# Kernel optimization log

Measured on AMD Instinct MI355X. Metric: run time of the kernel, lower is better.

## Reference

```python
import jax, jax.numpy as jnp
import numpy as np

T, B, D, H_DIM = 1024, 64, 512, 512
SIGMA = 0.01


def setup_inputs() -> dict:
    key = jax.random.key(0)
    ks = jax.random.split(key, 9)
    inp = {
        "inputs": jax.random.normal(ks[0], (T, B, D), dtype=jnp.float32),
        "W_xi": jax.random.normal(ks[1], (D, H_DIM), dtype=jnp.float32) * SIGMA,
        "W_hi": jax.random.normal(ks[2], (H_DIM, H_DIM), dtype=jnp.float32) * SIGMA,
        "b_i": jnp.zeros((H_DIM,), dtype=jnp.float32),
        "W_xf": jax.random.normal(ks[3], (D, H_DIM), dtype=jnp.float32) * SIGMA,
        "W_hf": jax.random.normal(ks[4], (H_DIM, H_DIM), dtype=jnp.float32) * SIGMA,
        "b_f": jnp.zeros((H_DIM,), dtype=jnp.float32),
        "W_xo": jax.random.normal(ks[5], (D, H_DIM), dtype=jnp.float32) * SIGMA,
        "W_ho": jax.random.normal(ks[6], (H_DIM, H_DIM), dtype=jnp.float32) * SIGMA,
        "b_o": jnp.zeros((H_DIM,), dtype=jnp.float32),
        "W_xc": jax.random.normal(ks[7], (D, H_DIM), dtype=jnp.float32) * SIGMA,
        "W_hc": jax.random.normal(ks[8], (H_DIM, H_DIM), dtype=jnp.float32) * SIGMA,
        "b_c": jnp.zeros((H_DIM,), dtype=jnp.float32),
    }
    return inp


def reference(inputs, W_xi, W_hi, b_i, W_xf, W_hf, b_f,
              W_xo, W_ho, b_o, W_xc, W_hc, b_c):
    # inputs: [T, B, D]. Precompute input-to-gate projections in one big
    # batched GEMM per gate (same math as per-step X @ W_x + b).
    Xi = jnp.einsum('tbd,dh->tbh', inputs, W_xi) + b_i
    Xf = jnp.einsum('tbd,dh->tbh', inputs, W_xf) + b_f
    Xo = jnp.einsum('tbd,dh->tbh', inputs, W_xo) + b_o
    Xc = jnp.einsum('tbd,dh->tbh', inputs, W_xc) + b_c

    Bsz = inputs.shape[1]
    H0 = jnp.zeros((Bsz, W_hi.shape[0]), dtype=inputs.dtype)
    C0 = jnp.zeros((Bsz, W_hi.shape[0]), dtype=inputs.dtype)

    def step(carry, xs):
        H, C = carry
        xi, xf, xo, xc = xs
        I = jax.nn.sigmoid(xi + H @ W_hi)
        F = jax.nn.sigmoid(xf + H @ W_hf)
        O = jax.nn.sigmoid(xo + H @ W_ho)
        C_tilde = jnp.tanh(xc + H @ W_hc)
        C = F * C + I * C_tilde
        H = O * jnp.tanh(C)
        return (H, C), H

    (H, C), outputs = jax.lax.scan(step, (H0, C0), (Xi, Xf, Xo, Xc))
    # outputs: [T, B, H] stacked hidden states (torch returns a list of them)
    return outputs, (H, C)
```

## Files before the change

kernel.cpp:

```cpp
#include <hip/hip_runtime.h>
#include <hip/hip_bf16.h>
#include <stdint.h>


typedef float    f32x4  __attribute__((ext_vector_type(4)));
typedef short    s16x8  __attribute__((ext_vector_type(8)));
typedef unsigned short u16;
typedef u16      u16x4  __attribute__((ext_vector_type(4)));
typedef unsigned int u32;

#define TT 1024
#define BB 64
#define DD 512
#define HH 512
#define NG 2048
#define NTEAM 8
#define NSLOT 8
#define NLW 128
#define NGEN 4

__device__ __forceinline__ u16 f2bf(float f) {
  __hip_bfloat16 h = __float2bfloat16(f);
  union { __hip_bfloat16 b; u16 u; } v; v.b = h; return v.u;
}
__device__ __forceinline__ float bf2f(u16 u) {
  union { unsigned int i; float f; } v; v.i = ((unsigned int)u) << 16; return v.f;
}
__device__ __forceinline__ float sig_fast(float x) {
  return 1.f / (1.f + __expf(-x));
}
__device__ __forceinline__ float tanh_fast(float x) {
  return 1.f - 2.f / (1.f + __expf(2.f * x));
}

__device__ __forceinline__ void gload_lds16(const u16* g, u16* l) {
  __builtin_amdgcn_global_load_lds(
      (const __attribute__((address_space(1))) unsigned int*)g,
      (__attribute__((address_space(3))) unsigned int*)l, 16, 0, 0);
}

__device__ __forceinline__ void st_plain(u32* p, u32 v) {
  asm volatile("global_store_dword %0, %1, off" :: "v"(p), "v"(v) : "memory");
}
__device__ __forceinline__ u32 ld_plain(const u32* p) {
  u32 v;
  asm volatile("global_load_dword %0, %1, off\n\ts_waitcnt vmcnt(0)"
               : "=v"(v) : "v"(p) : "memory");
  return v;
}

__global__ void k_cast(const float* __restrict__ in, u16* __restrict__ out, long n) {
  long i = ((long)blockIdx.x * blockDim.x + threadIdx.x) * 4;
  if (i >= n) return;
  const float4 v = *(const float4*)(in + i);
  u16x4 o; o.x = f2bf(v.x); o.y = f2bf(v.y); o.z = f2bf(v.z); o.w = f2bf(v.w);
  *(u16x4*)(out + i) = o;
}

__global__ void k_pack(const float* __restrict__ Wxi, const float* __restrict__ Whi, const float* __restrict__ bi,
                       const float* __restrict__ Wxf, const float* __restrict__ Whf, const float* __restrict__ bfi,
                       const float* __restrict__ Wxo, const float* __restrict__ Who, const float* __restrict__ bo,
                       const float* __restrict__ Wxc, const float* __restrict__ Whc, const float* __restrict__ bc,
                       u16* __restrict__ WxT, u16* __restrict__ WhT, float* __restrict__ biasp)
{
  const int k = blockIdx.x;
  const float* Wx[4] = {Wxi, Wxf, Wxo, Wxc};
  const float* Wh[4] = {Whi, Whf, Who, Whc};
  for (int h = threadIdx.x; h < HH; h += blockDim.x) {
#pragma unroll
    for (int g = 0; g < 4; ++g) {
      const long n = h * 4 + g;
      WxT[n * DD + k] = f2bf(Wx[g][(long)k * HH + h]);
      WhT[n * HH + k] = f2bf(Wh[g][(long)k * HH + h]);
    }
  }
  if (k == 0) {
    const float* bp[4] = {bi, bfi, bo, bc};
    for (int n = threadIdx.x; n < NG; n += blockDim.x)
      biasp[n] = bp[n & 3][n >> 2];
  }
}

__global__ __launch_bounds__(256) void k_gemm_x(
    const u16* __restrict__ A, const u16* __restrict__ BT,
    const float* __restrict__ biasp, u16* __restrict__ X)
{
  __shared__ __align__(16) u16 As[128 * 64];
  __shared__ __align__(16) u16 Bs[128 * 64];
  const int tid = threadIdx.x;
  const int l = tid & 63;
  const int w = tid >> 6;
  const int wr = w >> 1, wc = w & 1;
  const long brow = (long)blockIdx.y * 128;
  const int  bcol = blockIdx.x * 128;
  const int  lr = l >> 3, lc = l & 7;
  const int  cl = l & 15, rg = l >> 4;

  f32x4 acc[4][4];
#pragma unroll
  for (int m = 0; m < 4; ++m)
#pragma unroll
    for (int n = 0; n < 4; ++n) acc[m][n] = (f32x4){0.f, 0.f, 0.f, 0.f};

  for (int k0 = 0; k0 < DD; k0 += 64) {
#pragma unroll
    for (int j = 0; j < 4; ++j) {
      const int sub = w * 4 + j;
      gload_lds16(A  + (brow + sub * 8 + lr) * DD + k0 + lc * 8, &As[sub * 512]);
      gload_lds16(BT + ((long)(bcol + sub * 8 + lr)) * DD + k0 + lc * 8, &Bs[sub * 512]);
    }
    __syncthreads();
#pragma unroll
    for (int kk = 0; kk < 2; ++kk) {
      s16x8 af[4], bfr[4];
#pragma unroll
      for (int m = 0; m < 4; ++m)
        af[m] = *(const s16x8*)&As[(wr * 64 + m * 16 + cl) * 64 + kk * 32 + rg * 8];
#pragma unroll
      for (int n = 0; n < 4; ++n)
        bfr[n] = *(const s16x8*)&Bs[(wc * 64 + n * 16 + cl) * 64 + kk * 32 + rg * 8];
#pragma unroll
      for (int m = 0; m < 4; ++m)
#pragma unroll
        for (int n = 0; n < 4; ++n)
          acc[m][n] = __builtin_amdgcn_mfma_f32_16x16x32_bf16(af[m], bfr[n], acc[m][n], 0, 0, 0);
    }
    __syncthreads();
  }
#pragma unroll
  for (int n = 0; n < 4; ++n) {
    const int col = bcol + wc * 64 + n * 16 + cl;
    const float bv = biasp[col];
#pragma unroll
    for (int m = 0; m < 4; ++m)
#pragma unroll
      for (int j = 0; j < 4; ++j) {
        const long row = brow + wr * 64 + m * 16 + rg * 4 + j;
        X[row * NG + col] = f2bf(acc[m][n][j] + bv);
      }
  }
}

__global__ __launch_bounds__(512, 2) void k_lstm(
    const u16* __restrict__ X, const u16* __restrict__ WhT,
    u16* __restrict__ Hh, float* __restrict__ Cst,
    float* __restrict__ dout, float* __restrict__ doutH, float* __restrict__ doutC,
    u32* __restrict__ ctl, u32* __restrict__ flags, int t0, int t1)
{
  __shared__ __align__(16) float pre[8][260];
  __shared__ int s_team, s_slot, s_mixed;
  const int tid = threadIdx.x;

  if (tid == 0) {
    u32 x;
    asm volatile("s_getreg_b32 %0, hwreg(HW_REG_XCC_ID)" : "=s"(x));
    x &= 7u;
    u32 r = __hip_atomic_fetch_add(&ctl[x], 1u, __ATOMIC_RELAXED, __HIP_MEMORY_SCOPE_AGENT);
    u32 p = 0;
    if (r >= NSLOT)
      p = __hip_atomic_fetch_add(&ctl[8], 1u, __ATOMIC_RELAXED, __HIP_MEMORY_SCOPE_AGENT);
    __hip_atomic_fetch_add(&ctl[9], 1u, __ATOMIC_RELAXED, __HIP_MEMORY_SCOPE_AGENT);
    while (__hip_atomic_load(&ctl[9], __ATOMIC_RELAXED, __HIP_MEMORY_SCOPE_AGENT) < (u32)NLW)
      __builtin_amdgcn_s_sleep(4);
    u32 c[8];
#pragma unroll
    for (int i = 0; i < 8; ++i)
      c[i] = __hip_atomic_load(&ctl[i], __ATOMIC_RELAXED, __HIP_MEMORY_SCOPE_AGENT);
    int team = -1, slot = 0;
    if (r < NSLOT) { team = (int)x; slot = (int)r; }
    else {
      u32 acc = 0;
      for (int tt = 0; tt < 8; ++tt) {
        u32 have = c[tt] < NSLOT ? c[tt] : NSLOT;
        u32 miss = NSLOT - have;
        if (team < 0 && p < acc + miss) { team = tt; slot = (int)(have + (p - acc)); }
        acc += miss;
      }
    }
    s_team = team; s_slot = slot;
    s_mixed = (team >= 0 && c[team] < NSLOT) ? 1 : 0;
  }
  __syncthreads();
  const int team = s_team, slot = s_slot, mixed = s_mixed;
  if (team < 0) return;

  const int l = tid & 63, wv = tid >> 6;
  const int cl = l & 15, rg = l >> 4;
  const int gcol0 = slot * 256 + wv * 32;

  s16x8 bfr[2][16];
#pragma unroll
  for (int nt = 0; nt < 2; ++nt)
#pragma unroll
    for (int ks = 0; ks < 16; ++ks)
      bfr[nt][ks] = *(const s16x8*)&WhT[(long)(gcol0 + nt * 16 + cl) * HH + ks * 32 + rg * 8];

  const int prow = tid >> 6;
  const int phl  = tid & 63;
  const int grow = team * 8 + prow;
  const int ghl  = slot * 64 + phl;

  float creg;
  if (t0 == 0) creg = 0.f; else creg = Cst[grow * HH + ghl];

  u32* fteam = flags + (long)team * TT * NGEN * 32;

  for (int t = t0; t < t1; ++t) {
    const int s = t - t0;
    u16x4 xv = *(const u16x4*)&X[((long)s * BB + grow) * NG + slot * 256 + phl * 4];

    if (t > t0) {
      if (wv == 0) {
        u32* fstep = fteam + (long)(s - 1) * NGEN * 32;
        u32 vv; unsigned long long b;
        int g = 0;
        for (;;) {
          if (l < NSLOT) vv = ld_plain(fstep + g * 32 + l);
          else vv = 1u;
          b = __ballot(vv != 0);
          if (b == ~0ULL) break;
          ++g;
          if (g >= NGEN) break;
          __builtin_amdgcn_s_sleep(2);
        }
        while (b != ~0ULL) {
          __builtin_amdgcn_s_sleep(8);
          if (l < NSLOT)
            vv = __hip_atomic_load(fstep + l, __ATOMIC_RELAXED,
                                   __HIP_MEMORY_SCOPE_AGENT);
          else vv = 1u;
          b = __ballot(vv != 0);
        }
      }
      __syncthreads();
    }

    f32x4 a0a = (f32x4){0.f,0.f,0.f,0.f}, a0b = (f32x4){0.f,0.f,0.f,0.f};
    f32x4 a1a = (f32x4){0.f,0.f,0.f,0.f}, a1b = (f32x4){0.f,0.f,0.f,0.f};
    if (t > 0) {
      const u16* Hp = Hh + (long)(t - 1) * BB * HH;
      s16x8 af[16];
#pragma unroll
      for (int ks = 0; ks < 16; ++ks) af[ks] = (s16x8){0,0,0,0,0,0,0,0};
      if (cl < 8) {
#pragma unroll
        for (int ks = 0; ks < 16; ++ks)
          af[ks] = *(const s16x8*)&Hp[(team * 8 + cl) * HH + ks * 32 + rg * 8];
      }
#pragma unroll
      for (int ks = 0; ks < 16; ks += 2) {
        a0a = __builtin_amdgcn_mfma_f32_16x16x32_bf16(af[ks],     bfr[0][ks],     a0a, 0, 0, 0);
        a1a = __builtin_amdgcn_mfma_f32_16x16x32_bf16(af[ks],     bfr[1][ks],     a1a, 0, 0, 0);
        a0b = __builtin_amdgcn_mfma_f32_16x16x32_bf16(af[ks + 1], bfr[0][ks + 1], a0b, 0, 0, 0);
        a1b = __builtin_amdgcn_mfma_f32_16x16x32_bf16(af[ks + 1], bfr[1][ks + 1], a1b, 0, 0, 0);
      }
    }
    const f32x4 acc0 = a0a + a0b, acc1 = a1a + a1b;
    if (rg < 2) {
#pragma unroll
      for (int j = 0; j < 4; ++j) {
        pre[rg * 4 + j][wv * 32 + cl]      = acc0[j];
        pre[rg * 4 + j][wv * 32 + 16 + cl] = acc1[j];
      }
    }
    __syncthreads();

    f32x4 pv = *(const f32x4*)&pre[prow][phl * 4];
    const float pi = pv[0] + bf2f((u16)xv.x);
    const float pf = pv[1] + bf2f((u16)xv.y);
    const float po = pv[2] + bf2f((u16)xv.z);
    const float pc = pv[3] + bf2f((u16)xv.w);
    const float ig = sig_fast(pi);
    const float fg = sig_fast(pf);
    const float og = sig_fast(po);
    const float ct = tanh_fast(pc);
    creg = fg * creg + ig * ct;
    const float hv = og * tanh_fast(creg);
    const u16 hb = f2bf(hv);
    u16* hdst = &Hh[((long)t * BB + grow) * HH + ghl];
    if (!mixed) *hdst = hb;
    else asm volatile("global_store_short %0, %1, off sc1"
                      :: "v"(hdst), "v"((u32)hb) : "memory");

    asm volatile("s_waitcnt vmcnt(0)" ::: "memory");
    __syncthreads();
    if (tid == 0) {
      u32* fb = fteam + (long)s * NGEN * 32 + slot;
      if (!mixed) {
#pragma unroll
        for (int g = 0; g < NGEN; ++g) st_plain(fb + g * 32, 1u);
      } else {
#pragma unroll
        for (int g = 0; g < NGEN; ++g)
          __hip_atomic_store(fb + g * 32, 1u, __ATOMIC_RELAXED,
                             __HIP_MEMORY_SCOPE_AGENT);
      }
    }
    dout[((long)t * BB + grow) * HH + ghl] = hv;
    if (t == TT - 1) {
      doutH[grow * HH + ghl] = hv;
      doutC[grow * HH + ghl] = creg;
    }
  }

  Cst[grow * HH + ghl] = creg;
}

extern "C" void kernel_launch(void* const* d_in, const int* in_sizes, int n_in,
                              void* d_out, int out_size, void* d_ws, size_t ws_size,
                              hipStream_t stream)
{
  const float* inputs = (const float*)d_in[0];
  const float* W_xi = (const float*)d_in[1];
  const float* W_hi = (const float*)d_in[2];
  const float* b_i  = (const float*)d_in[3];
  const float* W_xf = (const float*)d_in[4];
  const float* W_hf = (const float*)d_in[5];
  const float* b_f  = (const float*)d_in[6];
  const float* W_xo = (const float*)d_in[7];
  const float* W_ho = (const float*)d_in[8];
  const float* b_o  = (const float*)d_in[9];
  const float* W_xc = (const float*)d_in[10];
  const float* W_hc = (const float*)d_in[11];
  const float* b_c  = (const float*)d_in[12];
  float* out = (float*)d_out;
  char* ws = (char*)d_ws;

  size_t off = 0;
  auto walloc = [&](size_t sz) { size_t o = off; off = (off + sz + 255) & ~(size_t)255; return o; };
  const size_t o_inbf  = walloc((size_t)TT * BB * DD * 2);
  const size_t o_WxT   = walloc((size_t)NG * DD * 2);
  const size_t o_WhT   = walloc((size_t)NG * HH * 2);
  const size_t o_bias  = walloc((size_t)NG * 4);
  const size_t o_C     = walloc((size_t)BB * HH * 4);
  const size_t o_Hh    = walloc((size_t)TT * BB * HH * 2);
  const size_t o_ctl   = walloc(256);
  const size_t flags_bytes = (size_t)NTEAM * TT * NGEN * 32 * 4;
  const size_t o_flags = walloc(flags_bytes);
  const size_t o_X     = off;

  const size_t bytes_per_step = (size_t)BB * NG * 2;
  long spc = (ws_size > o_X) ? (long)((ws_size - o_X) / bytes_per_step) : 0;
  if (spc > TT) spc = TT;
  spc &= ~1L;
  if (spc < 2) spc = 2;

  u16*   inbf  = (u16*)(ws + o_inbf);
  u16*   WxT   = (u16*)(ws + o_WxT);
  u16*   WhT   = (u16*)(ws + o_WhT);
  float* biasp = (float*)(ws + o_bias);
  u16*   Xbuf  = (u16*)(ws + o_X);
  u16*   Hh    = (u16*)(ws + o_Hh);
  float* Cst   = (float*)(ws + o_C);

  k_cast<<<dim3((TT * BB * DD) / 1024), dim3(256), 0, stream>>>(inputs, inbf, (long)TT * BB * DD);
  k_pack<<<dim3(DD), dim3(256), 0, stream>>>(W_xi, W_hi, b_i, W_xf, W_hf, b_f,
                                             W_xo, W_ho, b_o, W_xc, W_hc, b_c,
                                             WxT, WhT, biasp);

  float* doutH = out + (size_t)TT * BB * HH;
  float* doutC = doutH + (size_t)BB * HH;

  for (int t0 = 0; t0 < TT; t0 += (int)spc) {
    int t1 = t0 + (int)spc; if (t1 > TT) t1 = TT;
    const int rows = (t1 - t0) * BB;
    k_gemm_x<<<dim3(NG / 128, rows / 128), dim3(256), 0, stream>>>(
        inbf + (size_t)t0 * BB * DD, WxT, biasp, Xbuf);
    hipMemsetAsync(ws + o_ctl, 0, 256, stream);
    hipMemsetAsync(ws + o_flags, 0, flags_bytes, stream);
    k_lstm<<<dim3(NLW), dim3(512), 0, stream>>>(
        Xbuf, WhT, Hh, Cst, out, doutH, doutC,
        (u32*)(ws + o_ctl), (u32*)(ws + o_flags), t0, t1);
  }
}
```

Baseline: 4.379 ms.

## Fuse input-projection GEMM and LSTM recurrence into one producer-consumer persistent kernel

Replaces the separate X-projection GEMM and recurrent LSTM launches with one persistent kernel. 64 workgroups run the recurrence, and 192 workgroups compute GEMM tiles chunk by chunk, signalling per-chunk counters that the recurrence waits on. This lets the large input GEMM overlap with the latency-bound sequential scan. After finishing, the GEMM workers spin on dummy FMA work until the recurrence completes, presumably to keep clocks up or hold CUs. The change needs a full-size X buffer and relies on all 256 workgroups being co-resident.

Result: faster. 4.131 ms (-5.7%).

```diff
diff --git a/kernel.cpp b/kernel.cpp
--- a/kernel.cpp
+++ b/kernel.cpp
@@ -16,8 +16,13 @@
 #define NG 2048
 #define NTEAM 8
 #define NSLOT 8
-#define NLW 128
+#define NTWG 64
+#define NGWG 192
 #define NGEN 4
+#define CHUNK_STEPS 32
+#define NCHUNK 32
+#define TPC 256
+#define NTILES 8192
 
 __device__ __forceinline__ u16 f2bf(float f) {
   __hip_bfloat16 h = __float2bfloat16(f);
@@ -26,19 +31,14 @@
 __device__ __forceinline__ float bf2f(u16 u) {
   union { unsigned int i; float f; } v; v.i = ((unsigned int)u) << 16; return v.f;
 }
-__device__ __forceinline__ float sig_fast(float x) {
-  return 1.f / (1.f + __expf(-x));
-}
-__device__ __forceinline__ float tanh_fast(float x) {
-  return 1.f - 2.f / (1.f + __expf(2.f * x));
-}
+__device__ __forceinline__ float sig_fast(float x) { return 1.f / (1.f + __expf(-x)); }
+__device__ __forceinline__ float tanh_fast(float x) { return 1.f - 2.f / (1.f + __expf(2.f * x)); }
 
 __device__ __forceinline__ void gload_lds16(const u16* g, u16* l) {
   __builtin_amdgcn_global_load_lds(
       (const __attribute__((address_space(1))) unsigned int*)g,
       (__attribute__((address_space(3))) unsigned int*)l, 16, 0, 0);
 }
-
 __device__ __forceinline__ void st_plain(u32* p, u32 v) {
   asm volatile("global_store_dword %0, %1, off" :: "v"(p), "v"(v) : "memory");
 }
@@ -47,6 +47,9 @@
   asm volatile("global_load_dword %0, %1, off\n\ts_waitcnt vmcnt(0)"
                : "=v"(v) : "v"(p) : "memory");
   return v;
+}
+__device__ __forceinline__ void st_short_sc1(u16* p, u16 v) {
+  asm volatile("global_store_short %0, %1, off sc1" :: "v"(p), "v"((u32)v) : "memory");
 }
 
 __global__ void k_cast(const float* __restrict__ in, u16* __restrict__ out, long n) {
@@ -81,75 +84,94 @@
   }
 }
 
-__global__ __launch_bounds__(256) void k_gemm_x(
-    const u16* __restrict__ A, const u16* __restrict__ BT,
-    const float* __restrict__ biasp, u16* __restrict__ X)
+__global__ __launch_bounds__(512, 2) void k_fused(
+    const u16* __restrict__ inbf, const u16* __restrict__ WxT,
+    const u16* __restrict__ WhT, const float* __restrict__ biasp,
+    u16* __restrict__ X, u16* __restrict__ Hh, float* __restrict__ Cst,
+    float* __restrict__ dout, float* __restrict__ doutH, float* __restrict__ doutC,
+    u32* __restrict__ ctl, u32* __restrict__ flags, u32* __restrict__ cnt)
 {
   __shared__ __align__(16) u16 As[128 * 64];
   __shared__ __align__(16) u16 Bs[128 * 64];
-  const int tid = threadIdx.x;
-  const int l = tid & 63;
-  const int w = tid >> 6;
-  const int wr = w >> 1, wc = w & 1;
-  const long brow = (long)blockIdx.y * 128;
-  const int  bcol = blockIdx.x * 128;
-  const int  lr = l >> 3, lc = l & 7;
-  const int  cl = l & 15, rg = l >> 4;
-
-  f32x4 acc[4][4];
-#pragma unroll
-  for (int m = 0; m < 4; ++m)
-#pragma unroll
-    for (int n = 0; n < 4; ++n) acc[m][n] = (f32x4){0.f, 0.f, 0.f, 0.f};
-
-  for (int k0 = 0; k0 < DD; k0 += 64) {
-#pragma unroll
-    for (int j = 0; j < 4; ++j) {
-      const int sub = w * 4 + j;
-      gload_lds16(A  + (brow + sub * 8 + lr) * DD + k0 + lc * 8, &As[sub * 512]);
-      gload_lds16(BT + ((long)(bcol + sub * 8 + lr)) * DD + k0 + lc * 8, &Bs[sub * 512]);
-    }
-    __syncthreads();
-#pragma unroll
-    for (int kk = 0; kk < 2; ++kk) {
-      s16x8 af[4], bfr[4];
-#pragma unroll
-      for (int m = 0; m < 4; ++m)
-        af[m] = *(const s16x8*)&As[(wr * 64 + m * 16 + cl) * 64 + kk * 32 + rg * 8];
-#pragma unroll
-      for (int n = 0; n < 4; ++n)
-        bfr[n] = *(const s16x8*)&Bs[(wc * 64 + n * 16 + cl) * 64 + kk * 32 + rg * 8];
-#pragma unroll
-      for (int m = 0; m < 4; ++m)
-#pragma unroll
-        for (int n = 0; n < 4; ++n)
-          acc[m][n] = __builtin_amdgcn_mfma_f32_16x16x32_bf16(af[m], bfr[n], acc[m][n], 0, 0, 0);
-    }
-    __syncthreads();
-  }
-#pragma unroll
-  for (int n = 0; n < 4; ++n) {
-    const int col = bcol + wc * 64 + n * 16 + cl;
-    const float bv = biasp[col];
-#pragma unroll
-    for (int m = 0; m < 4; ++m)
-#pragma unroll
-      for (int j = 0; j < 4; ++j) {
-        const long row = brow + wr * 64 + m * 16 + rg * 4 + j;
-        X[row * NG + col] = f2bf(acc[m][n][j] + bv);
-      }
-  }
-}
-
-__global__ __launch_bounds__(512, 2) void k_lstm(
-    const u16* __restrict__ X, const u16* __restrict__ WhT,
-    u16* __restrict__ Hh, float* __restrict__ Cst,
-    float* __restrict__ dout, float* __restrict__ doutH, float* __restrict__ doutC,
-    u32* __restrict__ ctl, u32* __restrict__ flags, int t0, int t1)
-{
   __shared__ __align__(16) float pre[8][260];
   __shared__ int s_team, s_slot, s_mixed;
   const int tid = threadIdx.x;
+  const int role = blockIdx.x;
+  const int l = tid & 63, wv = tid >> 6;
+
+  if (role >= NTWG) {
+    const int gwg = role - NTWG;
+    const int wr = wv >> 2, wc = wv & 3;
+    const int lr = l >> 3, lc = l & 7;
+    const int cl = l & 15, rg = l >> 4;
+
+    for (int tile = gwg; tile < NTILES; tile += NGWG) {
+      const int c = tile >> 8, q = tile & 255;
+      const long brow = (long)(c * 16 + (q >> 4)) * 128;
+      const int  bcol = (q & 15) * 128;
+
+      f32x4 acc[4][2];
+#pragma unroll
+      for (int m = 0; m < 4; ++m)
+#pragma unroll
+        for (int n = 0; n < 2; ++n) acc[m][n] = (f32x4){0.f, 0.f, 0.f, 0.f};
+
+      for (int k0 = 0; k0 < DD; k0 += 64) {
+#pragma unroll
+        for (int j = 0; j < 2; ++j) {
+          const int sub = wv * 2 + j;
+          gload_lds16(inbf + (brow + sub * 8 + lr) * DD + k0 + lc * 8, &As[sub * 512]);
+          gload_lds16(WxT  + ((long)(bcol + sub * 8 + lr)) * DD + k0 + lc * 8, &Bs[sub * 512]);
+        }
+        __syncthreads();
+#pragma unroll
+        for (int kk = 0; kk < 2; ++kk) {
+          s16x8 af[4], bfx[2];
+#pragma unroll
+          for (int m = 0; m < 4; ++m)
+            af[m] = *(const s16x8*)&As[(wr * 64 + m * 16 + cl) * 64 + kk * 32 + rg * 8];
+#pragma unroll
+          for (int n = 0; n < 2; ++n)
+            bfx[n] = *(const s16x8*)&Bs[(wc * 32 + n * 16 + cl) * 64 + kk * 32 + rg * 8];
+#pragma unroll
+          for (int m = 0; m < 4; ++m)
+#pragma unroll
+            for (int n = 0; n < 2; ++n)
+              acc[m][n] = __builtin_amdgcn_mfma_f32_16x16x32_bf16(af[m], bfx[n], acc[m][n], 0, 0, 0);
+        }
+        __syncthreads();
+      }
+#pragma unroll
+      for (int n = 0; n < 2; ++n) {
+        const int col = bcol + wc * 32 + n * 16 + cl;
+        const float bv = biasp[col];
+#pragma unroll
+        for (int m = 0; m < 4; ++m)
+#pragma unroll
+          for (int j = 0; j < 4; ++j) {
+            const long row = brow + wr * 64 + m * 16 + rg * 4 + j;
+            st_short_sc1(&X[row * NG + col], f2bf(acc[m][n][j] + bv));
+          }
+      }
+      asm volatile("s_waitcnt vmcnt(0)" ::: "memory");
+      __syncthreads();
+      if (tid == 0)
+        __hip_atomic_fetch_add(&cnt[c * 32], 1u, __ATOMIC_RELAXED, __HIP_MEMORY_SCOPE_AGENT);
+      __syncthreads();
+    }
+    float hacc = 1.0f + (float)tid;
+    int it2 = 0;
+    for (;;) {
+#pragma unroll
+      for (int u = 0; u < 64; ++u) hacc = __builtin_fmaf(hacc, 1.0000001f, 1.0e-7f);
+      asm volatile("" :: "v"(hacc));
+      if ((++it2 & 63) == 0) {
+        if (__hip_atomic_load(&ctl[16], __ATOMIC_RELAXED, __HIP_MEMORY_SCOPE_AGENT) >= (u32)NTWG)
+          break;
+      }
+    }
+    return;
+  }
 
   if (tid == 0) {
     u32 x;
@@ -160,7 +182,7 @@
     if (r >= NSLOT)
       p = __hip_atomic_fetch_add(&ctl[8], 1u, __ATOMIC_RELAXED, __HIP_MEMORY_SCOPE_AGENT);
     __hip_atomic_fetch_add(&ctl[9], 1u, __ATOMIC_RELAXED, __HIP_MEMORY_SCOPE_AGENT);
-    while (__hip_atomic_load(&ctl[9], __ATOMIC_RELAXED, __HIP_MEMORY_SCOPE_AGENT) < (u32)NLW)
+    while (__hip_atomic_load(&ctl[9], __ATOMIC_RELAXED, __HIP_MEMORY_SCOPE_AGENT) < (u32)NTWG)
       __builtin_amdgcn_s_sleep(4);
     u32 c[8];
 #pragma unroll
@@ -184,7 +206,6 @@
   const int team = s_team, slot = s_slot, mixed = s_mixed;
   if (team < 0) return;
 
-  const int l = tid & 63, wv = tid >> 6;
   const int cl = l & 15, rg = l >> 4;
   const int gcol0 = slot * 256 + wv * 32;
 
@@ -200,110 +221,116 @@
   const int grow = team * 8 + prow;
   const int ghl  = slot * 64 + phl;
 
-  float creg;
-  if (t0 == 0) creg = 0.f; else creg = Cst[grow * HH + ghl];
-
+  float creg = 0.f;
   u32* fteam = flags + (long)team * TT * NGEN * 32;
 
-  for (int t = t0; t < t1; ++t) {
-    const int s = t - t0;
-    u16x4 xv = *(const u16x4*)&X[((long)s * BB + grow) * NG + slot * 256 + phl * 4];
-
-    if (t > t0) {
-      if (wv == 0) {
-        u32* fstep = fteam + (long)(s - 1) * NGEN * 32;
-        u32 vv; unsigned long long b;
-        int g = 0;
-        for (;;) {
-          if (l < NSLOT) vv = ld_plain(fstep + g * 32 + l);
-          else vv = 1u;
-          b = __ballot(vv != 0);
-          if (b == ~0ULL) break;
-          ++g;
-          if (g >= NGEN) break;
-          __builtin_amdgcn_s_sleep(2);
-        }
-        while (b != ~0ULL) {
-          __builtin_amdgcn_s_sleep(8);
-          if (l < NSLOT)
-            vv = __hip_atomic_load(fstep + l, __ATOMIC_RELAXED,
-                                   __HIP_MEMORY_SCOPE_AGENT);
-          else vv = 1u;
-          b = __ballot(vv != 0);
+  for (int c = 0; c < NCHUNK; ++c) {
+    if (tid == 0) {
+      while (__hip_atomic_load(&cnt[c * 32], __ATOMIC_RELAXED, __HIP_MEMORY_SCOPE_AGENT) < (u32)TPC)
+        __builtin_amdgcn_s_sleep(16);
+    }
+    __syncthreads();
+
+    for (int t = c * CHUNK_STEPS; t < (c + 1) * CHUNK_STEPS; ++t) {
+      u16x4 xv = *(const u16x4*)&X[((long)t * BB + grow) * NG + slot * 256 + phl * 4];
+
+      if (t > 0) {
+        if (wv == 0) {
+          u32* fstep = fteam + (long)(t - 1) * NGEN * 32;
+          u32 vv; unsigned long long b;
+          int g = 0;
+          for (;;) {
+            if (l < NSLOT) vv = ld_plain(fstep + g * 32 + l);
+            else vv = 1u;
+            b = __ballot(vv != 0);
+            if (b == ~0ULL) break;
+            ++g;
+            if (g >= NGEN) break;
+            __builtin_amdgcn_s_sleep(2);
+          }
+          while (b != ~0ULL) {
+            __builtin_amdgcn_s_sleep(8);
+            if (l < NSLOT)
+              vv = __hip_atomic_load(fstep + l, __ATOMIC_RELAXED, __HIP_MEMORY_SCOPE_AGENT);
+            else vv = 1u;
+            b = __ballot(vv != 0);
+          }
+        }
+        __syncthreads();
+      }
+
+      f32x4 a0a = (f32x4){0.f,0.f,0.f,0.f}, a0b = (f32x4){0.f,0.f,0.f,0.f};
+      f32x4 a1a = (f32x4){0.f,0.f,0.f,0.f}, a1b = (f32x4){0.f,0.f,0.f,0.f};
+      if (t > 0) {
+        const u16* Hp = Hh + (long)(t - 1) * BB * HH;
+        s16x8 af[16];
+#pragma unroll
+        for (int ks = 0; ks < 16; ++ks) af[ks] = (s16x8){0,0,0,0,0,0,0,0};
+        if (cl < 8) {
+#pragma unroll
+          for (int ks = 0; ks < 16; ++ks)
+            af[ks] = *(const s16x8*)&Hp[(team * 8 + cl) * HH + ks * 32 + rg * 8];
+        }
+#pragma unroll
+        for (int ks = 0; ks < 16; ks += 2) {
+          a0a = __builtin_amdgcn_mfma_f32_16x16x32_bf16(af[ks],     bfr[0][ks],     a0a, 0, 0, 0);
+          a1a = __builtin_amdgcn_mfma_f32_16x16x32_bf16(af[ks],     bfr[1][ks],     a1a, 0, 0, 0);
+          a0b = __builtin_amdgcn_mfma_f32_16x16x32_bf16(af[ks + 1], bfr[0][ks + 1], a0b, 0, 0, 0);
+          a1b = __builtin_amdgcn_mfma_f32_16x16x32_bf16(af[ks + 1], bfr[1][ks + 1], a1b, 0, 0, 0);
+        }
+      }
+      const f32x4 acc0 = a0a + a0b, acc1 = a1a + a1b;
+      if (rg < 2) {
+#pragma unroll
+        for (int j = 0; j < 4; ++j) {
+          pre[rg * 4 + j][wv * 32 + cl]      = acc0[j];
+          pre[rg * 4 + j][wv * 32 + 16 + cl] = acc1[j];
         }
       }
       __syncthreads();
-    }
-
-    f32x4 a0a = (f32x4){0.f,0.f,0.f,0.f}, a0b = (f32x4){0.f,0.f,0.f,0.f};
-    f32x4 a1a = (f32x4){0.f,0.f,0.f,0.f}, a1b = (f32x4){0.f,0.f,0.f,0.f};
-    if (t > 0) {
-      const u16* Hp = Hh + (long)(t - 1) * BB * HH;
-      s16x8 af[16];
-#pragma unroll
-      for (int ks = 0; ks < 16; ++ks) af[ks] = (s16x8){0,0,0,0,0,0,0,0};
-      if (cl < 8) {
-#pragma unroll
-        for (int ks = 0; ks < 16; ++ks)
-          af[ks] = *(const s16x8*)&Hp[(team * 8 + cl) * HH + ks * 32 + rg * 8];
-      }
-#pragma unroll
-      for (int ks = 0; ks < 16; ks += 2) {
-        a0a = __builtin_amdgcn_mfma_f32_16x16x32_bf16(af[ks],     bfr[0][ks],     a0a, 0, 0, 0);
-        a1a = __builtin_amdgcn_mfma_f32_16x16x32_bf16(af[ks],     bfr[1][ks],     a1a, 0, 0, 0);
-        a0b = __builtin_amdgcn_mfma_f32_16x16x32_bf16(af[ks + 1], bfr[0][ks + 1], a0b, 0, 0, 0);
-        a1b = __builtin_amdgcn_mfma_f32_16x16x32_bf16(af[ks + 1], bfr[1][ks + 1], a1b, 0, 0, 0);
-      }
-    }
-    const f32x4 acc0 = a0a + a0b, acc1 = a1a + a1b;
-    if (rg < 2) {
-#pragma unroll
-      for (int j = 0; j < 4; ++j) {
-        pre[rg * 4 + j][wv * 32 + cl]      = acc0[j];
-        pre[rg * 4 + j][wv * 32 + 16 + cl] = acc1[j];
-      }
-    }
-    __syncthreads();
-
-    f32x4 pv = *(const f32x4*)&pre[prow][phl * 4];
-    const float pi = pv[0] + bf2f((u16)xv.x);
-    const float pf = pv[1] + bf2f((u16)xv.y);
-    const float po = pv[2] + bf2f((u16)xv.z);
-    const float pc = pv[3] + bf2f((u16)xv.w);
-    const float ig = sig_fast(pi);
-    const float fg = sig_fast(pf);
-    const float og = sig_fast(po);
-    const float ct = tanh_fast(pc);
-    creg = fg * creg + ig * ct;
-    const float hv = og * tanh_fast(creg);
-    const u16 hb = f2bf(hv);
-    u16* hdst = &Hh[((long)t * BB + grow) * HH + ghl];
-    if (!mixed) *hdst = hb;
-    else asm volatile("global_store_short %0, %1, off sc1"
-                      :: "v"(hdst), "v"((u32)hb) : "memory");
-
-    asm volatile("s_waitcnt vmcnt(0)" ::: "memory");
-    __syncthreads();
-    if (tid == 0) {
-      u32* fb = fteam + (long)s * NGEN * 32 + slot;
-      if (!mixed) {
-#pragma unroll
-        for (int g = 0; g < NGEN; ++g) st_plain(fb + g * 32, 1u);
-      } else {
-#pragma unroll
-        for (int g = 0; g < NGEN; ++g)
-          __hip_atomic_store(fb + g * 32, 1u, __ATOMIC_RELAXED,
-                             __HIP_MEMORY_SCOPE_AGENT);
-      }
-    }
-    dout[((long)t * BB + grow) * HH + ghl] = hv;
-    if (t == TT - 1) {
-      doutH[grow * HH + ghl] = hv;
-      doutC[grow * HH + ghl] = creg;
+
+      f32x4 pv = *(const f32x4*)&pre[prow][phl * 4];
+      const float pi = pv[0] + bf2f((u16)xv.x);
+      const float pf = pv[1] + bf2f((u16)xv.y);
+      const float po = pv[2] + bf2f((u16)xv.z);
+      const float pc = pv[3] + bf2f((u16)xv.w);
+      const float ig = sig_fast(pi);
+      const float fg = sig_fast(pf);
+      const float og = sig_fast(po);
+      const float ct = tanh_fast(pc);
+      creg = fg * creg + ig * ct;
+      const float hv = og * tanh_fast(creg);
+      const u16 hb = f2bf(hv);
+      u16* hdst = &Hh[((long)t * BB + grow) * HH + ghl];
+      if (!mixed) *hdst = hb;
+      else asm volatile("global_store_short %0, %1, off sc1"
+                        :: "v"(hdst), "v"((u32)hb) : "memory");
+
+      asm volatile("s_waitcnt vmcnt(0)" ::: "memory");
+      __syncthreads();
+      if (tid == 0) {
+        u32* fb = fteam + (long)t * NGEN * 32 + slot;
+        if (!mixed) {
+#pragma unroll
+          for (int g = 0; g < NGEN; ++g) st_plain(fb + g * 32, 1u);
+        } else {
+#pragma unroll
+          for (int g = 0; g < NGEN; ++g)
+            __hip_atomic_store(fb + g * 32, 1u, __ATOMIC_RELAXED, __HIP_MEMORY_SCOPE_AGENT);
+        }
+      }
+      dout[((long)t * BB + grow) * HH + ghl] = hv;
+      if (t == TT - 1) {
+        doutH[grow * HH + ghl] = hv;
+        doutC[grow * HH + ghl] = creg;
+      }
     }
   }
 
   Cst[grow * HH + ghl] = creg;
+  __syncthreads();
+  if (tid == 0)
+    __hip_atomic_fetch_add(&ctl[16], 1u, __ATOMIC_RELAXED, __HIP_MEMORY_SCOPE_AGENT);
 }
 
 extern "C" void kernel_launch(void* const* d_in, const int* in_sizes, int n_in,
@@ -337,13 +364,8 @@
   const size_t o_ctl   = walloc(256);
   const size_t flags_bytes = (size_t)NTEAM * TT * NGEN * 32 * 4;
   const size_t o_flags = walloc(flags_bytes);
-  const size_t o_X     = off;
-
-  const size_t bytes_per_step = (size_t)BB * NG * 2;
-  long spc = (ws_size > o_X) ? (long)((ws_size - o_X) / bytes_per_step) : 0;
-  if (spc > TT) spc = TT;
-  spc &= ~1L;
-  if (spc < 2) spc = 2;
+  const size_t o_cnt   = walloc((size_t)NCHUNK * 32 * 4);
+  const size_t o_X     = walloc((size_t)TT * BB * NG * 2);
 
   u16*   inbf  = (u16*)(ws + o_inbf);
   u16*   WxT   = (u16*)(ws + o_WxT);
@@ -361,15 +383,11 @@
   float* doutH = out + (size_t)TT * BB * HH;
   float* doutC = doutH + (size_t)BB * HH;
 
-  for (int t0 = 0; t0 < TT; t0 += (int)spc) {
-    int t1 = t0 + (int)spc; if (t1 > TT) t1 = TT;
-    const int rows = (t1 - t0) * BB;
-    k_gemm_x<<<dim3(NG / 128, rows / 128), dim3(256), 0, stream>>>(
-        inbf + (size_t)t0 * BB * DD, WxT, biasp, Xbuf);
-    hipMemsetAsync(ws + o_ctl, 0, 256, stream);
-    hipMemsetAsync(ws + o_flags, 0, flags_bytes, stream);
-    k_lstm<<<dim3(NLW), dim3(512), 0, stream>>>(
-        Xbuf, WhT, Hh, Cst, out, doutH, doutC,
-        (u32*)(ws + o_ctl), (u32*)(ws + o_flags), t0, t1);
-  }
-}
+  hipMemsetAsync(ws + o_ctl, 0, 256, stream);
+  hipMemsetAsync(ws + o_flags, 0, flags_bytes, stream);
+  hipMemsetAsync(ws + o_cnt, 0, (size_t)NCHUNK * 32 * 4, stream);
+
+  k_fused<<<dim3(NTWG + NGWG), dim3(512), 0, stream>>>(
+      inbf, WxT, WhT, biasp, Xbuf, Hh, Cst, out, doutH, doutC,
+      (u32*)(ws + o_ctl), (u32*)(ws + o_flags), (u32*)(ws + o_cnt));
+}
```
